# Optimization experiments

Measured on AMD Instinct MI355X. Metric: run time of the kernel, lower is better.

## Reference

```python
import jax, jax.numpy as jnp
import numpy as np

N = 100_000       # nodes
E = 1_600_000     # edges (avg degree 16)
FE = 32           # edge feature dim (in_channels_e)
FX = 128          # node feature dim (in_channels_x)
OX = 128          # out_channels_x
OE = 128          # out_channels_e


def setup_inputs() -> dict:
    key = jax.random.key(0)
    k1, k2, k3, k4, k5, k6, k7 = jax.random.split(key, 7)
    x = jax.random.normal(k1, (N, FX), dtype=jnp.float32)
    edge_index = jax.random.randint(k2, (2, E), 0, N, dtype=jnp.int64)
    edge_attr = jax.random.normal(k3, (E, FE), dtype=jnp.float32)
    # Linear params (torch nn.Linear: y = x @ W.T + b); store W already transposed.
    sx = 1.0 / np.sqrt(FX)
    se = 1.0 / np.sqrt(FE)
    Wx = jax.random.uniform(k4, (FX, OX), minval=-sx, maxval=sx, dtype=jnp.float32)
    bx = jax.random.uniform(k5, (OX,), minval=-sx, maxval=sx, dtype=jnp.float32)
    We = jax.random.uniform(k6, (FE, OE), minval=-se, maxval=se, dtype=jnp.float32)
    be = jax.random.uniform(k7, (OE,), minval=-se, maxval=se, dtype=jnp.float32)
    return {"x": x, "edge_index": edge_index, "edge_attr": edge_attr,
            "Wx": Wx, "bx": bx, "We": We, "be": be}


def reference(x, edge_index, edge_attr, Wx, bx, We, be):
    # torch: adj = to_dense(sparse_coo(edge_index, edge_attr)); adj.sum(dim=1)
    # == segment-sum of edge_attr over the row index edge_index[0].  O(E*Fe)
    # instead of the O(N*N*Fe) dense materialization.
    agg = jax.ops.segment_sum(edge_attr, edge_index[0], num_segments=x.shape[0])  # [N, FE]
    hx = x @ Wx + bx      # [N, OX]
    he = agg @ We + be    # [N, OE]
    return jax.nn.relu(jnp.concatenate([hx, he], axis=1))  # [N, OX+OE]
```

## Files before the change

kernel.cpp:

```cpp
#include <hip/hip_runtime.h>
#include <hip/hip_bf16.h>

#define NN     100000
#define EE     1600000
#define FE     32
#define FX     128
#define OX     128
#define OE     128
#define OUTC   (OX + OE)
#define NTILES (NN / 16)

#define NPP     128
#define NPART   782
#define PSTRIDE 2816
#define PCPAD   16

#define AGG_BYTES   12800000UL
#define FLAG_OFF    12800000UL
#define PCUR_OFF    12800256UL
#define PBUF_OFF    12850432UL
#define SBUF_OFF    21658880UL
#define PACK_OFF    30467328UL
#define WS_NEED     (PACK_OFF + (size_t)NN * 4)

typedef unsigned short u16;
typedef short            shortx8  __attribute__((ext_vector_type(8)));
typedef float            floatx4  __attribute__((ext_vector_type(4)));
typedef int              intx4    __attribute__((ext_vector_type(4)));

__device__ __forceinline__ u16 f2b(float f) {
    union { float f; unsigned u; } v; v.f = f;
    unsigned u = v.u;
    return (u16)((u + 0x7FFFu + ((u >> 16) & 1u)) >> 16);
}

__global__ __launch_bounds__(256) void init_kernel(
    int* __restrict__ pcur, int* __restrict__ flag, const int* __restrict__ ei) {
    int gid = blockIdx.x * 256 + threadIdx.x;
    if (gid * 4 < NPART * PCPAD) {
        intx4 z = {0, 0, 0, 0};
        *(intx4*)(pcur + gid * 4) = z;
    }
    if (gid == 0) {
        int orv = 0;
        for (int j = 1; j < 256; j += 2) orv |= ei[j];
        *flag = (orv == 0) ? 1 : 0;
    }
}

__global__ __launch_bounds__(512) void part_kernel(
    const int* __restrict__ ei, const int* __restrict__ flag,
    int* __restrict__ pcur, int* __restrict__ pbuf) {
    __shared__ int h[NPART];
    __shared__ int gb[NPART];
    int tid = threadIdx.x;
    for (int i = tid; i < NPART; i += 512) h[i] = 0;
    __syncthreads();
    int is64 = *flag;
    int e0 = blockIdx.x * 8192;
    int rows[16];
#pragma unroll
    for (int i = 0; i < 16; ++i) {
        int e = e0 + i * 512 + tid;
        int row = -1;
        if (e < EE) row = is64 ? ei[2 * (size_t)e] : ei[e];
        rows[i] = ((unsigned)row < (unsigned)NN) ? row : -1;
        if (rows[i] >= 0) atomicAdd(&h[rows[i] >> 7], 1);
    }
    __syncthreads();
    for (int b = tid; b < NPART; b += 512) {
        int c = h[b];
        gb[b] = c ? atomicAdd(pcur + b * PCPAD, c) : 0;
    }
    __syncthreads();
#pragma unroll
    for (int i = 0; i < 16; ++i) {
        int row = rows[i];
        if (row >= 0) {
            int e = e0 + i * 512 + tid;
            int p = row >> 7;
            int off = atomicAdd(&gb[p], 1);
            if (off < PSTRIDE)
                pbuf[(size_t)p * PSTRIDE + off] = ((row & 127) << 21) | e;
        }
    }
}

__global__ __launch_bounds__(256) void sort_kernel(
    const int* __restrict__ pcur, const int* __restrict__ pbuf,
    int* __restrict__ sbuf, int* __restrict__ pack) {
    __shared__ int hist[NPP];
    __shared__ int boff[NPP];
    __shared__ int cur[NPP];
    int tid = threadIdx.x;
    int p = blockIdx.x;
    if (tid < NPP) hist[tid] = 0;
    int cnt = pcur[p * PCPAD];
    if (cnt > PSTRIDE) cnt = PSTRIDE;
    const int* seg = pbuf + (size_t)p * PSTRIDE;
    __syncthreads();
#pragma unroll 4
    for (int i = tid; i < cnt; i += 256)
        atomicAdd(&hist[((unsigned)seg[i]) >> 21], 1);
    __syncthreads();
    if (tid < 64) {
        int a = hist[2 * tid], b = hist[2 * tid + 1];
        int s = a + b;
        int pre = s;
#pragma unroll
        for (int off = 1; off < 64; off <<= 1) {
            int t = __shfl_up(pre, off, 64);
            if (tid >= off) pre += t;
        }
        boff[2 * tid]     = pre - s;
        boff[2 * tid + 1] = pre - b;
        cur[2 * tid]      = pre - s;
        cur[2 * tid + 1]  = pre - b;
    }
    __syncthreads();
    int* dst = sbuf + (size_t)p * PSTRIDE;
#pragma unroll 4
    for (int i = tid; i < cnt; i += 256) {
        int en = seg[i];
        int o = atomicAdd(&cur[((unsigned)en) >> 21], 1);
        dst[o] = en;
    }
    if (tid < NPP) {
        int node = p * NPP + tid;
        if (node < NN) {
            int d = hist[tid];
            if (d > 127) d = 127;
            unsigned off = (unsigned)(p * PSTRIDE + boff[tid]);
            pack[node] = (int)((off << 7) | (unsigned)d);
        }
    }
}

__global__ __launch_bounds__(256) void gather_kernel(
    const int* __restrict__ pack, const int* __restrict__ sbuf,
    const float* __restrict__ ea, float* __restrict__ agg) {
    __shared__ int ids[4][128];
    int wave = threadIdx.x >> 6, lane = threadIdx.x & 63;
    int node = blockIdx.x * 4 + wave;
    int pk = pack[node];
    int off = (int)(((unsigned)pk) >> 7);
    int deg = pk & 127;
    for (int j = lane; j < deg; j += 64)
        ids[wave][j] = sbuf[off + j] & 0x1FFFFF;
    __syncthreads();

    int g = lane >> 3, sub = lane & 7;
    floatx4 acc0 = {0.f, 0.f, 0.f, 0.f};
    floatx4 acc1 = {0.f, 0.f, 0.f, 0.f};
    int j = g;
    for (; j + 8 < deg; j += 16) {
        acc0 += *(const floatx4*)(ea + (size_t)ids[wave][j] * FE + sub * 4);
        acc1 += *(const floatx4*)(ea + (size_t)ids[wave][j + 8] * FE + sub * 4);
    }
    if (j < deg)
        acc0 += *(const floatx4*)(ea + (size_t)ids[wave][j] * FE + sub * 4);
    acc0 += acc1;

#pragma unroll
    for (int m = 8; m <= 32; m <<= 1) {
#pragma unroll
        for (int c = 0; c < 4; ++c)
            acc0[c] += __shfl_xor(acc0[c], m, 64);
    }
    if (g == 0)
        *(floatx4*)(agg + (size_t)node * FE + sub * 4) = acc0;
}

__global__ __launch_bounds__(256) void zero_probe_kernel(
    float* __restrict__ agg, int* __restrict__ flag, const int* __restrict__ ei) {
    int gid = blockIdx.x * 256 + threadIdx.x;
    floatx4 z = {0.f, 0.f, 0.f, 0.f};
    *(floatx4*)(agg + (size_t)gid * 4) = z;
    if (gid == 0) {
        int orv = 0;
        for (int j = 1; j < 256; j += 2) orv |= ei[j];
        *flag = (orv == 0) ? 1 : 0;
    }
}

__global__ __launch_bounds__(256) void scatter_kernel(
    const int* __restrict__ rows, const float* __restrict__ ea,
    float* __restrict__ agg, const int* __restrict__ flag) {
    int gid = blockIdx.x * 256 + threadIdx.x;
    int e  = gid >> 3;
    int fg = (gid & 7) << 2;
    int is64 = *flag;
    int row = is64 ? rows[2 * (size_t)e] : rows[e];
    floatx4 v = *(const floatx4*)(ea + (size_t)e * FE + fg);
    float* dst = agg + (size_t)row * FE + fg;
#pragma unroll
    for (int j = 0; j < 4; ++j) unsafeAtomicAdd(dst + j, v[j]);
}

__global__ __launch_bounds__(256) void fused_gemm_kernel(
    const float* __restrict__ x, const float* __restrict__ agg,
    const float* __restrict__ Wx, const float* __restrict__ bx,
    const float* __restrict__ We, const float* __restrict__ be,
    float* __restrict__ out, int nwaves) {
    __shared__ short fragWx[32][64][8];
    __shared__ short fragWe[8][64][8];

    int tid = threadIdx.x;

    for (int c = tid; c < (FX * OX) / 4; c += 256) {
        int base = c * 4;
        int k = base >> 7;
        int n = base & 127;
        floatx4 v = *(const floatx4*)(Wx + base);
        int kt = k >> 5, jj = k & 7, halfk = (k >> 3) & 3;
#pragma unroll
        for (int u = 0; u < 4; ++u) {
            int nn = n + u;
            fragWx[kt * 8 + (nn >> 4)][halfk * 16 + (nn & 15)][jj] = (short)f2b(v[u]);
        }
    }
    for (int c = tid; c < (FE * OE) / 4; c += 256) {
        int base = c * 4;
        int k = base >> 7;
        int n = base & 127;
        floatx4 v = *(const floatx4*)(We + base);
        int jj = k & 7, halfk = (k >> 3) & 3;
#pragma unroll
        for (int u = 0; u < 4; ++u) {
            int nn = n + u;
            fragWe[nn >> 4][halfk * 16 + (nn & 15)][jj] = (short)f2b(v[u]);
        }
    }
    __syncthreads();

    int wave = tid >> 6, lane = tid & 63;
    int q = lane >> 4, i = lane & 15;

    shortx8 bwe[8];
    float bxv[8], bev[8];
#pragma unroll
    for (int nt = 0; nt < 8; ++nt) {
        bwe[nt] = *(const shortx8*)&fragWe[nt][lane][0];
        bxv[nt] = bx[nt * 16 + i];
        bev[nt] = be[nt * 16 + i];
    }

    int gwave = blockIdx.x * 4 + wave;
    for (int mt = gwave; mt < NTILES; mt += nwaves) {
        int m0 = mt << 4;
        int arow = m0 + i;

        const float* xp = x + (size_t)arow * FX + q * 8;
        shortx8 ax[4];
#pragma unroll
        for (int kt = 0; kt < 4; ++kt) {
            floatx4 a0 = *(const floatx4*)(xp + kt * 32);
            floatx4 a1 = *(const floatx4*)(xp + kt * 32 + 4);
#pragma unroll
            for (int j = 0; j < 4; ++j) {
                ax[kt][j]     = (short)f2b(a0[j]);
                ax[kt][4 + j] = (short)f2b(a1[j]);
            }
        }

        const float* ap = agg + (size_t)arow * FE + q * 8;
        floatx4 g0 = *(const floatx4*)ap;
        floatx4 g1 = *(const floatx4*)(ap + 4);
        shortx8 aagg;
#pragma unroll
        for (int j = 0; j < 4; ++j) {
            aagg[j]     = (short)f2b(g0[j]);
            aagg[4 + j] = (short)f2b(g1[j]);
        }

#pragma unroll
        for (int nt = 0; nt < 8; ++nt) {
            floatx4 acc = {0.f, 0.f, 0.f, 0.f};
#pragma unroll
            for (int kt = 0; kt < 4; ++kt) {
                shortx8 b = *(const shortx8*)&fragWx[kt * 8 + nt][lane][0];
                acc = __builtin_amdgcn_mfma_f32_16x16x32_bf16(ax[kt], b, acc, 0, 0, 0);
            }
            floatx4 acche = {0.f, 0.f, 0.f, 0.f};
            acche = __builtin_amdgcn_mfma_f32_16x16x32_bf16(aagg, bwe[nt], acche, 0, 0, 0);
#pragma unroll
            for (int r = 0; r < 4; ++r) {
                int orow = m0 + q * 4 + r;
                float* op = out + (size_t)orow * OUTC + nt * 16 + i;
                float h = acc[r] + bxv[nt];
                op[0]  = h > 0.f ? h : 0.f;
                float g = acche[r] + bev[nt];
                op[OX] = g > 0.f ? g : 0.f;
            }
        }
    }
}

extern "C" void kernel_launch(void* const* d_in, const int* in_sizes, int n_in,
                              void* d_out, int out_size, void* d_ws, size_t ws_size,
                              hipStream_t stream) {
    const float* x  = (const float*)d_in[0];
    const int*   ei = (const int*)d_in[1];
    const float* ea = (const float*)d_in[2];
    const float* Wx = (const float*)d_in[3];
    const float* bx = (const float*)d_in[4];
    const float* We = (const float*)d_in[5];
    const float* be = (const float*)d_in[6];
    float* out = (float*)d_out;

    float* agg  = (float*)d_ws;
    int*   flagC= (int*)((char*)d_ws + FLAG_OFF);
    int*   pcur = (int*)((char*)d_ws + PCUR_OFF);
    int*   pbuf = (int*)((char*)d_ws + PBUF_OFF);
    int*   sbuf = (int*)((char*)d_ws + SBUF_OFF);
    int*   pack = (int*)((char*)d_ws + PACK_OFF);

    if (ws_size >= WS_NEED) {
        init_kernel<<<(NPART * PCPAD / 4 + 255) / 256, 256, 0, stream>>>(pcur, flagC, ei);
        part_kernel<<<(EE + 8191) / 8192, 512, 0, stream>>>(ei, flagC, pcur, pbuf);
        sort_kernel<<<NPART, 256, 0, stream>>>(pcur, pbuf, sbuf, pack);
        gather_kernel<<<NN / 4, 256, 0, stream>>>(pack, sbuf, ea, agg);
    } else {
        int* flagA = (int*)((char*)d_ws + AGG_BYTES);
        zero_probe_kernel<<<(NN * FE) / 4 / 256, 256, 0, stream>>>(agg, flagA, ei);
        scatter_kernel<<<(EE * 8) / 256, 256, 0, stream>>>(ei, ea, agg, flagA);
    }

    const int blocks = 1563;
    fused_gemm_kernel<<<blocks, 256, 0, stream>>>(x, agg, Wx, bx, We, be, out,
                                                  blocks * 4);
}
```

Measured before the change: 449.3 us.

## Prepack bf16 weight fragments once, gather edges without LDS, widen partition blocks

Adds a prep kernel that converts Wx/We to bf16 MFMA fragment layout once in workspace. The GEMM kernel then reads B fragments from global memory instead of having each of 1563 blocks rebuild them in LDS. The gather kernel drops the shared-memory id staging and its barrier, and loads up to four edge ids per lane directly, with four independent accumulators. The partition kernel moves to 1024-thread blocks. The trade-off is extra global/L2 traffic for weight fragments inside the GEMM loop and one more kernel launch. The old LDS GEMM is kept as a fallback when the workspace is small.

Measured after the change: 425.8 us. 5.2% less time.

```diff
diff --git a/kernel.cpp b/kernel.cpp
--- a/kernel.cpp
+++ b/kernel.cpp
@@ -21,7 +21,9 @@
 #define PBUF_OFF    12850432UL
 #define SBUF_OFF    21658880UL
 #define PACK_OFF    30467328UL
-#define WS_NEED     (PACK_OFF + (size_t)NN * 4)
+#define WBUF_OFF    30867328UL
+#define WFE_ELEMS   (32 * 64 * 8)
+#define WS_NEED     (WBUF_OFF + 73728UL)
 
 typedef unsigned short u16;
 typedef short            shortx8  __attribute__((ext_vector_type(8)));
@@ -48,36 +50,69 @@
     }
 }
 
-__global__ __launch_bounds__(512) void part_kernel(
+__global__ __launch_bounds__(256) void prep_kernel(
+    const float* __restrict__ Wx, const float* __restrict__ We,
+    short* __restrict__ wbuf) {
+    int c = blockIdx.x * 256 + threadIdx.x;
+    short* wfx = wbuf;
+    short* wfe = wbuf + WFE_ELEMS;
+    if (c < (FX * OX) / 4) {
+        int base = c * 4;
+        int k = base >> 7;
+        int n = base & 127;
+        floatx4 v = *(const floatx4*)(Wx + base);
+        int kt = k >> 5, jj = k & 7, halfk = (k >> 3) & 3;
+#pragma unroll
+        for (int u = 0; u < 4; ++u) {
+            int nn = n + u;
+            wfx[((kt * 8 + (nn >> 4)) * 64 + halfk * 16 + (nn & 15)) * 8 + jj] =
+                (short)f2b(v[u]);
+        }
+    } else if (c < (FX * OX) / 4 + (FE * OE) / 4) {
+        int base = (c - (FX * OX) / 4) * 4;
+        int k = base >> 7;
+        int n = base & 127;
+        floatx4 v = *(const floatx4*)(We + base);
+        int jj = k & 7, halfk = (k >> 3) & 3;
+#pragma unroll
+        for (int u = 0; u < 4; ++u) {
+            int nn = n + u;
+            wfe[((nn >> 4) * 64 + halfk * 16 + (nn & 15)) * 8 + jj] =
+                (short)f2b(v[u]);
+        }
+    }
+}
+
+__global__ __launch_bounds__(1024) void part_kernel(
     const int* __restrict__ ei, const int* __restrict__ flag,
     int* __restrict__ pcur, int* __restrict__ pbuf) {
     __shared__ int h[NPART];
     __shared__ int gb[NPART];
     int tid = threadIdx.x;
-    for (int i = tid; i < NPART; i += 512) h[i] = 0;
+    if (tid < NPART) h[tid] = 0;
     __syncthreads();
     int is64 = *flag;
     int e0 = blockIdx.x * 8192;
-    int rows[16];
-#pragma unroll
-    for (int i = 0; i < 16; ++i) {
-        int e = e0 + i * 512 + tid;
+    int rows[8];
+#pragma unroll
+    for (int i = 0; i < 8; ++i) {
+        int e = e0 + i * 1024 + tid;
         int row = -1;
         if (e < EE) row = is64 ? ei[2 * (size_t)e] : ei[e];
         rows[i] = ((unsigned)row < (unsigned)NN) ? row : -1;
         if (rows[i] >= 0) atomicAdd(&h[rows[i] >> 7], 1);
     }
     __syncthreads();
-    for (int b = tid; b < NPART; b += 512) {
-        int c = h[b];
-        gb[b] = c ? atomicAdd(pcur + b * PCPAD, c) : 0;
-    }
-    __syncthreads();
-#pragma unroll
-    for (int i = 0; i < 16; ++i) {
+    if (tid < NPART) {
+        int c = h[tid];
+        gb[tid] = c ? atomicAdd(pcur + tid * PCPAD, c) : 0;
+    }
+    __syncthreads();
+#pragma unroll
+    for (int i = 0; i < 8; ++i) {
         int row = rows[i];
         if (row >= 0) {
-            int e = e0 + i * 512 + tid;
+            int e = e0 + i * 1024 + tid;
             int p = row >> 7;
             int off = atomicAdd(&gb[p], 1);
             if (off < PSTRIDE)
@@ -139,27 +174,30 @@
 __global__ __launch_bounds__(256) void gather_kernel(
     const int* __restrict__ pack, const int* __restrict__ sbuf,
     const float* __restrict__ ea, float* __restrict__ agg) {
-    __shared__ int ids[4][128];
-    int wave = threadIdx.x >> 6, lane = threadIdx.x & 63;
-    int node = blockIdx.x * 4 + wave;
+    int lane = threadIdx.x & 63;
+    int node = (blockIdx.x * 256 + threadIdx.x) >> 6;
     int pk = pack[node];
     int off = (int)(((unsigned)pk) >> 7);
     int deg = pk & 127;
-    for (int j = lane; j < deg; j += 64)
-        ids[wave][j] = sbuf[off + j] & 0x1FFFFF;
-    __syncthreads();
-
     int g = lane >> 3, sub = lane & 7;
-    floatx4 acc0 = {0.f, 0.f, 0.f, 0.f};
-    floatx4 acc1 = {0.f, 0.f, 0.f, 0.f};
-    int j = g;
-    for (; j + 8 < deg; j += 16) {
-        acc0 += *(const floatx4*)(ea + (size_t)ids[wave][j] * FE + sub * 4);
-        acc1 += *(const floatx4*)(ea + (size_t)ids[wave][j + 8] * FE + sub * 4);
-    }
-    if (j < deg)
-        acc0 += *(const floatx4*)(ea + (size_t)ids[wave][j] * FE + sub * 4);
-    acc0 += acc1;
+
+    int e0 = -1, e1 = -1, e2 = -1, e3 = -1;
+    if (g      < deg) e0 = sbuf[off + g]      & 0x1FFFFF;
+    if (g + 8  < deg) e1 = sbuf[off + g + 8]  & 0x1FFFFF;
+    if (g + 16 < deg) e2 = sbuf[off + g + 16] & 0x1FFFFF;
+    if (g + 24 < deg) e3 = sbuf[off + g + 24] & 0x1FFFFF;
+
+    floatx4 z = {0.f, 0.f, 0.f, 0.f};
+    floatx4 acc0 = z, acc1 = z, acc2 = z, acc3 = z;
+    if (e0 >= 0) acc0 = *(const floatx4*)(ea + (size_t)e0 * FE + sub * 4);
+    if (e1 >= 0) acc1 = *(const floatx4*)(ea + (size_t)e1 * FE + sub * 4);
+    if (e2 >= 0) acc2 = *(const floatx4*)(ea + (size_t)e2 * FE + sub * 4);
+    if (e3 >= 0) acc3 = *(const floatx4*)(ea + (size_t)e3 * FE + sub * 4);
+    for (int j = g + 32; j < deg; j += 8) {
+        int e = sbuf[off + j] & 0x1FFFFF;
+        acc0 += *(const floatx4*)(ea + (size_t)e * FE + sub * 4);
+    }
+    acc0 += acc1; acc2 += acc3; acc0 += acc2;
 
 #pragma unroll
     for (int m = 8; m <= 32; m <<= 1) {
@@ -199,14 +237,82 @@
 
 __global__ __launch_bounds__(256) void fused_gemm_kernel(
     const float* __restrict__ x, const float* __restrict__ agg,
+    const short* __restrict__ wbuf, const float* __restrict__ bx,
+    const float* __restrict__ be, float* __restrict__ out, int nwaves) {
+    const short* wfx = wbuf;
+    const short* wfe = wbuf + WFE_ELEMS;
+    int tid = threadIdx.x;
+    int wave = tid >> 6, lane = tid & 63;
+    int q = lane >> 4, i = lane & 15;
+
+    shortx8 bwe[8];
+    float bxv[8], bev[8];
+#pragma unroll
+    for (int nt = 0; nt < 8; ++nt) {
+        bwe[nt] = *(const shortx8*)(wfe + ((size_t)nt * 64 + lane) * 8);
+        bxv[nt] = bx[nt * 16 + i];
+        bev[nt] = be[nt * 16 + i];
+    }
+
+    int gwave = blockIdx.x * 4 + wave;
+    for (int mt = gwave; mt < NTILES; mt += nwaves) {
+        int m0 = mt << 4;
+        int arow = m0 + i;
+
+        const float* xp = x + (size_t)arow * FX + q * 8;
+        shortx8 ax[4];
+#pragma unroll
+        for (int kt = 0; kt < 4; ++kt) {
+            floatx4 a0 = *(const floatx4*)(xp + kt * 32);
+            floatx4 a1 = *(const floatx4*)(xp + kt * 32 + 4);
+#pragma unroll
+            for (int j = 0; j < 4; ++j) {
+                ax[kt][j]     = (short)f2b(a0[j]);
+                ax[kt][4 + j] = (short)f2b(a1[j]);
+            }
+        }
+
+        const float* ap = agg + (size_t)arow * FE + q * 8;
+        floatx4 g0 = *(const floatx4*)ap;
+        floatx4 g1 = *(const floatx4*)(ap + 4);
+        shortx8 aagg;
+#pragma unroll
+        for (int j = 0; j < 4; ++j) {
+            aagg[j]     = (short)f2b(g0[j]);
+            aagg[4 + j] = (short)f2b(g1[j]);
+        }
+
+#pragma unroll
+        for (int nt = 0; nt < 8; ++nt) {
+            floatx4 acc = {0.f, 0.f, 0.f, 0.f};
+#pragma unroll
+            for (int kt = 0; kt < 4; ++kt) {
+                shortx8 b = *(const shortx8*)(wfx + (((size_t)kt * 8 + nt) * 64 + lane) * 8);
+                acc = __builtin_amdgcn_mfma_f32_16x16x32_bf16(ax[kt], b, acc, 0, 0, 0);
+            }
+            floatx4 acche = {0.f, 0.f, 0.f, 0.f};
+            acche = __builtin_amdgcn_mfma_f32_16x16x32_bf16(aagg, bwe[nt], acche, 0, 0, 0);
+#pragma unroll
+            for (int r = 0; r < 4; ++r) {
+                int orow = m0 + q * 4 + r;
+                float* op = out + (size_t)orow * OUTC + nt * 16 + i;
+                float h = acc[r] + bxv[nt];
+                op[0]  = h > 0.f ? h : 0.f;
+                float g = acche[r] + bev[nt];
+                op[OX] = g > 0.f ? g : 0.f;
+            }
+        }
+    }
+}
+
+__global__ __launch_bounds__(256) void fused_gemm_lds_kernel(
+    const float* __restrict__ x, const float* __restrict__ agg,
     const float* __restrict__ Wx, const float* __restrict__ bx,
     const float* __restrict__ We, const float* __restrict__ be,
     float* __restrict__ out, int nwaves) {
     __shared__ short fragWx[32][64][8];
     __shared__ short fragWe[8][64][8];
-
     int tid = threadIdx.x;
-
     for (int c = tid; c < (FX * OX) / 4; c += 256) {
         int base = c * 4;
         int k = base >> 7;
@@ -232,10 +338,8 @@
         }
     }
     __syncthreads();
-
     int wave = tid >> 6, lane = tid & 63;
     int q = lane >> 4, i = lane & 15;
-
     shortx8 bwe[8];
     float bxv[8], bev[8];
 #pragma unroll
@@ -244,12 +348,10 @@
         bxv[nt] = bx[nt * 16 + i];
         bev[nt] = be[nt * 16 + i];
     }
-
     int gwave = blockIdx.x * 4 + wave;
     for (int mt = gwave; mt < NTILES; mt += nwaves) {
         int m0 = mt << 4;
         int arow = m0 + i;
-
         const float* xp = x + (size_t)arow * FX + q * 8;
         shortx8 ax[4];
 #pragma unroll
@@ -262,7 +364,6 @@
                 ax[kt][4 + j] = (short)f2b(a1[j]);
             }
         }
-
         const float* ap = agg + (size_t)arow * FE + q * 8;
         floatx4 g0 = *(const floatx4*)ap;
         floatx4 g1 = *(const floatx4*)(ap + 4);
@@ -272,7 +373,6 @@
             aagg[j]     = (short)f2b(g0[j]);
             aagg[4 + j] = (short)f2b(g1[j]);
         }
-
 #pragma unroll
         for (int nt = 0; nt < 8; ++nt) {
             floatx4 acc = {0.f, 0.f, 0.f, 0.f};
@@ -314,19 +414,23 @@
     int*   pbuf = (int*)((char*)d_ws + PBUF_OFF);
     int*   sbuf = (int*)((char*)d_ws + SBUF_OFF);
     int*   pack = (int*)((char*)d_ws + PACK_OFF);
+    short* wbuf = (short*)((char*)d_ws + WBUF_OFF);
+
+    const int blocks = 1563;
 
     if (ws_size >= WS_NEED) {
+        prep_kernel<<<20, 256, 0, stream>>>(Wx, We, wbuf);
         init_kernel<<<(NPART * PCPAD / 4 + 255) / 256, 256, 0, stream>>>(pcur, flagC, ei);
-        part_kernel<<<(EE + 8191) / 8192, 512, 0, stream>>>(ei, flagC, pcur, pbuf);
+        part_kernel<<<(EE + 8191) / 8192, 1024, 0, stream>>>(ei, flagC, pcur, pbuf);
         sort_kernel<<<NPART, 256, 0, stream>>>(pcur, pbuf, sbuf, pack);
         gather_kernel<<<NN / 4, 256, 0, stream>>>(pack, sbuf, ea, agg);
+        fused_gemm_kernel<<<blocks, 256, 0, stream>>>(x, agg, wbuf, bx, be, out,
+                                                      blocks * 4);
     } else {
         int* flagA = (int*)((char*)d_ws + AGG_BYTES);
         zero_probe_kernel<<<(NN * FE) / 4 / 256, 256, 0, stream>>>(agg, flagA, ei);
         scatter_kernel<<<(EE * 8) / 256, 256, 0, stream>>>(ei, ea, agg, flagA);
-    }
-
-    const int blocks = 1563;
-    fused_gemm_kernel<<<blocks, 256, 0, stream>>>(x, agg, Wx, bx, We, be, out,
-                                                  blocks * 4);
-}
+        fused_gemm_lds_kernel<<<blocks, 256, 0, stream>>>(x, agg, Wx, bx, We, be,
+                                                          out, blocks * 4);
+    }
+}
```
